# Kernel tuning notes

Hardware: AMD Instinct MI355X
Metric: run time of the kernel (lower is better)

The kernel has to match this reference:

```python
import jax, jax.numpy as jnp
import numpy as np
import math


def setup_inputs() -> dict:
    key = jax.random.key(0)
    k1, k2, k3 = jax.random.split(key, 3)
    B, L, H, E = 2, 2048, 8, 64
    queries = jax.random.normal(k1, (B, L, H, E), dtype=jnp.float32)
    keys = jax.random.normal(k2, (B, L, H, E), dtype=jnp.float32)
    values = jax.random.normal(k3, (B, L, H, E), dtype=jnp.float32)
    return {"queries": queries, "keys": keys, "values": values}


def reference(queries, keys, values):
    B, L, H, E = queries.shape
    scale = 1.0 / math.sqrt(E)
    # [B,H,L,S] attention scores
    scores = jnp.einsum('blhe,bshe->bhls', queries, keys)
    # causal mask: positions s > l masked to -inf (scale * -inf stays -inf)
    causal = jnp.triu(jnp.ones((L, L), dtype=bool), k=1)  # True above diagonal
    scores = jnp.where(causal[None, None, :, :], -jnp.inf, scores)
    attn = scale * scores
    SA = jax.nn.softmax(attn, axis=-1)  # dropout p=0.0 -> identity
    V = jnp.einsum('bhls,bshd->blhd', SA, values)
    return (V, SA)
```

## Files before the change

kernel.cpp:

```cpp
#include <hip/hip_runtime.h>
#include <math.h>

#define L_DIM 2048
#define H_DIM 8
#define ROWSTRIDE 512
#define NT 512
#define QSCALE 0.18033688011112042f

typedef __attribute__((ext_vector_type(8))) short short8;
typedef __attribute__((ext_vector_type(4))) float floatx4;

__device__ __forceinline__ unsigned short f2bf(float f) {
    unsigned int u = __builtin_bit_cast(unsigned int, f);
    return (unsigned short)((u + 0x8000u) >> 16);
}

__device__ __forceinline__ float fexp2(float x) {
#if __has_builtin(__builtin_amdgcn_exp2f)
    return __builtin_amdgcn_exp2f(x);
#else
    return exp2f(x);
#endif
}

__device__ __forceinline__ short8 pack8(float4 a, float4 b) {
    union { unsigned short us[8]; short8 v; } pk;
    pk.us[0]=f2bf(a.x); pk.us[1]=f2bf(a.y); pk.us[2]=f2bf(a.z); pk.us[3]=f2bf(a.w);
    pk.us[4]=f2bf(b.x); pk.us[5]=f2bf(b.y); pk.us[6]=f2bf(b.z); pk.us[7]=f2bf(b.w);
    return pk.v;
}

__device__ __forceinline__ short8 pack8q(float4 a, float4 b) {
    union { unsigned short us[8]; short8 v; } pk;
    pk.us[0]=f2bf(a.x*QSCALE); pk.us[1]=f2bf(a.y*QSCALE);
    pk.us[2]=f2bf(a.z*QSCALE); pk.us[3]=f2bf(a.w*QSCALE);
    pk.us[4]=f2bf(b.x*QSCALE); pk.us[5]=f2bf(b.y*QSCALE);
    pk.us[6]=f2bf(b.z*QSCALE); pk.us[7]=f2bf(b.w*QSCALE);
    return pk.v;
}

__device__ __forceinline__ int swz(int row, int col) {
    return (row << 6) + ((((col >> 3) ^ (row & 7)) << 3) | (col & 7));
}

__global__ __launch_bounds__(NT, 4)
void attn_mfma4(const float* __restrict__ Q, const float* __restrict__ K,
                const float* __restrict__ Vv, float* __restrict__ outV,
                float* __restrict__ outSA)
{
    __shared__ __align__(16) unsigned char smem[41984];
    unsigned short* Ks = (unsigned short*)(smem);
    unsigned short* Vt = (unsigned short*)(smem + 16384);
    unsigned short* Ps = (unsigned short*)(smem + 32768);
    float* Ml = (float*)(smem + 40960);
    float* Ll = (float*)(smem + 41472);
    float* Ob = (float*)(smem);

    const int t    = threadIdx.x;
    const int lane = t & 63;
    const int w    = t >> 6;
    const int g    = w >> 2;
    const int wg   = w & 3;
    const int l15  = lane & 15;
    const int quad = lane >> 4;
    const int gc   = g << 5;

    const int bid = blockIdx.x;
    const int c   = bid & 255;
    const int hf  = bid >> 8;
    const int bh  = c & 15;
    const int p   = c >> 4;
    const int qt  = hf ? p : (31 - p);
    const int h   = bh & 7;
    const int b   = bh >> 3;
    const int q0  = qt << 6;
    const int ntiles = qt + 1;

    const float* Qb = Q  + (size_t)b * L_DIM * ROWSTRIDE + h * 64;
    const float* Kb = K  + (size_t)b * L_DIM * ROWSTRIDE + h * 64;
    const float* Vb = Vv + (size_t)b * L_DIM * ROWSTRIDE + h * 64;
    float* saBase = outSA + (size_t)(b * H_DIM + h) * L_DIM * L_DIM;

    const int sr = t >> 3, sc = (t & 7) << 3;
    const int kswz = swz(sr, sc);

    short8 aQ0, aQ1;
    {
        const float* qsrc = Qb + (size_t)(q0 + 16 * wg + l15) * ROWSTRIDE + quad * 8;
        aQ0 = pack8q(*(const float4*)(qsrc),      *(const float4*)(qsrc + 4));
        aQ1 = pack8q(*(const float4*)(qsrc + 32), *(const float4*)(qsrc + 36));
    }

    float m_r[4], l_r[4];
#pragma unroll
    for (int r = 0; r < 4; ++r) { m_r[r] = -INFINITY; l_r[r] = 0.f; }

    {
        const float* src = Kb + (size_t)sr * ROWSTRIDE + sc;
        *(short8*)&Ks[kswz] = pack8(*(const float4*)src, *(const float4*)(src + 4));
    }
    __syncthreads();

    for (int st = 0; st < ntiles; ++st) {
        const int cur = st & 1;
        const int stp = (st + 1 < ntiles) ? (st + 1) : st;
        const float* ksrc = Kb + (size_t)((stp << 6) + sr) * ROWSTRIDE + sc;
        float4 kf0 = *(const float4*)(ksrc);
        float4 kf1 = *(const float4*)(ksrc + 4);

        const unsigned short* Kc = Ks + (cur << 12);
        floatx4 d[2];
#pragma unroll
        for (int jj = 0; jj < 2; ++jj) {
            const int sb = gc + (jj << 4) + l15;
            short8 b0 = *(const short8*)&Kc[swz(sb, quad * 8)];
            short8 b1 = *(const short8*)&Kc[swz(sb, 32 + quad * 8)];
            floatx4 acc = {0.f, 0.f, 0.f, 0.f};
            acc = __builtin_amdgcn_mfma_f32_16x16x32_bf16(aQ0, b0, acc, 0, 0, 0);
            acc = __builtin_amdgcn_mfma_f32_16x16x32_bf16(aQ1, b1, acc, 0, 0, 0);
            d[jj] = acc;
        }
        const int s0 = st << 6;
        const bool diag = (st == qt);
#pragma unroll
        for (int r = 0; r < 4; ++r) {
            const int lrow = q0 + 16 * wg + quad * 4 + r;
            float v0 = d[0][r], v1 = d[1][r];
            if (diag) {
                v0 = (s0 + gc +  0 + l15 <= lrow) ? v0 : -INFINITY;
                v1 = (s0 + gc + 16 + l15 <= lrow) ? v1 : -INFINITY;
            }
            float vm = fmaxf(v0, v1);
#pragma unroll
            for (int mk = 1; mk < 16; mk <<= 1) vm = fmaxf(vm, __shfl_xor(vm, mk));
            const float mnew = fmaxf(m_r[r], vm);
            const float msafe = (mnew == -INFINITY) ? 0.0f : mnew;
            float es = fexp2(v0 - msafe) + fexp2(v1 - msafe);
#pragma unroll
            for (int mk = 1; mk < 16; mk <<= 1) es += __shfl_xor(es, mk);
            l_r[r] = l_r[r] * fexp2(m_r[r] - msafe) + es;
            m_r[r] = mnew;
        }
        if (st + 1 < ntiles)
            *(short8*)&Ks[((cur ^ 1) << 12) + kswz] = pack8(kf0, kf1);
        __syncthreads();
    }

    if (l15 == 0) {
#pragma unroll
        for (int r = 0; r < 4; ++r) {
            const int row = 16 * wg + quad * 4 + r;
            Ml[g * 64 + row] = m_r[r];
            Ll[g * 64 + row] = l_r[r];
        }
    }
    {
        const float* src = Kb + (size_t)sr * ROWSTRIDE + sc;
        *(short8*)&Ks[kswz] = pack8(*(const float4*)src, *(const float4*)(src + 4));
        const float* vsrc = Vb + (size_t)sr * ROWSTRIDE + sc;
        float4 f0 = *(const float4*)(vsrc);
        float4 f1 = *(const float4*)(vsrc + 4);
        Vt[swz(sc + 0, sr)] = f2bf(f0.x); Vt[swz(sc + 1, sr)] = f2bf(f0.y);
        Vt[swz(sc + 2, sr)] = f2bf(f0.z); Vt[swz(sc + 3, sr)] = f2bf(f0.w);
        Vt[swz(sc + 4, sr)] = f2bf(f1.x); Vt[swz(sc + 5, sr)] = f2bf(f1.y);
        Vt[swz(sc + 6, sr)] = f2bf(f1.z); Vt[swz(sc + 7, sr)] = f2bf(f1.w);
    }
    __syncthreads();

    float mfin[4], invl[4];
#pragma unroll
    for (int r = 0; r < 4; ++r) {
        const int row = 16 * wg + quad * 4 + r;
        float m0 = Ml[row], m1 = Ml[64 + row];
        float l0 = Ll[row], l1 = Ll[64 + row];
        float mf = fmaxf(m0, m1);
        float lf = l0 * fexp2(m0 - mf) + l1 * fexp2(m1 - mf);
        mfin[r] = mf;
        invl[r] = 1.0f / lf;
    }

    floatx4 oacc[4];
#pragma unroll
    for (int j = 0; j < 4; ++j) oacc[j] = (floatx4){0.f, 0.f, 0.f, 0.f};

    for (int st = 0; st < ntiles; ++st) {
        const int cur = st & 1;
        const int stp = (st + 1 < ntiles) ? (st + 1) : st;
        const float* ksrc = Kb + (size_t)((stp << 6) + sr) * ROWSTRIDE + sc;
        const float* vsrc = Vb + (size_t)((stp << 6) + sr) * ROWSTRIDE + sc;
        float4 kf0 = *(const float4*)(ksrc);
        float4 kf1 = *(const float4*)(ksrc + 4);
        float4 vf0 = *(const float4*)(vsrc);
        float4 vf1 = *(const float4*)(vsrc + 4);

        const unsigned short* Kc = Ks + (cur << 12);
        floatx4 d[2];
#pragma unroll
        for (int jj = 0; jj < 2; ++jj) {
            const int sb = gc + (jj << 4) + l15;
            short8 b0 = *(const short8*)&Kc[swz(sb, quad * 8)];
            short8 b1 = *(const short8*)&Kc[swz(sb, 32 + quad * 8)];
            floatx4 acc = {0.f, 0.f, 0.f, 0.f};
            acc = __builtin_amdgcn_mfma_f32_16x16x32_bf16(aQ0, b0, acc, 0, 0, 0);
            acc = __builtin_amdgcn_mfma_f32_16x16x32_bf16(aQ1, b1, acc, 0, 0, 0);
            d[jj] = acc;
        }
        const int s0 = st << 6;
        const bool diag = (st == qt);
#pragma unroll
        for (int r = 0; r < 4; ++r) {
            const int lrow = q0 + 16 * wg + quad * 4 + r;
            float* sap = saBase + (size_t)lrow * L_DIM + s0 + gc + l15;
            const float mr = mfin[r], il = invl[r];
#pragma unroll
            for (int jj = 0; jj < 2; ++jj) {
                float v = d[jj][r];
                bool ok = !diag || (s0 + gc + 16 * jj + l15 <= lrow);
                float pv = ok ? fexp2(v - mr) * il : 0.0f;
                sap[16 * jj] = pv;
                Ps[swz(16 * wg + quad * 4 + r, gc + 16 * jj + l15)] = f2bf(pv);
            }
        }
        short8 aP = *(const short8*)&Ps[swz(16 * wg + l15, gc + quad * 8)];
        const unsigned short* Vc = Vt + (cur << 12);
#pragma unroll
        for (int j = 0; j < 4; ++j) {
            short8 bv = *(const short8*)&Vc[swz(16 * j + l15, gc + quad * 8)];
            oacc[j] = __builtin_amdgcn_mfma_f32_16x16x32_bf16(aP, bv, oacc[j], 0, 0, 0);
        }
        if (st + 1 < ntiles) {
            const int nb = (cur ^ 1) << 12;
            *(short8*)&Ks[nb + kswz] = pack8(kf0, kf1);
            unsigned short* Vn = Vt + nb;
            Vn[swz(sc + 0, sr)] = f2bf(vf0.x); Vn[swz(sc + 1, sr)] = f2bf(vf0.y);
            Vn[swz(sc + 2, sr)] = f2bf(vf0.z); Vn[swz(sc + 3, sr)] = f2bf(vf0.w);
            Vn[swz(sc + 4, sr)] = f2bf(vf1.x); Vn[swz(sc + 5, sr)] = f2bf(vf1.y);
            Vn[swz(sc + 6, sr)] = f2bf(vf1.z); Vn[swz(sc + 7, sr)] = f2bf(vf1.w);
        }
        __syncthreads();
    }

    if (g == 1) {
#pragma unroll
        for (int r = 0; r < 4; ++r) {
            const int row = 16 * wg + quad * 4 + r;
#pragma unroll
            for (int j = 0; j < 4; ++j)
                Ob[row * 65 + 16 * j + l15] = oacc[j][r];
        }
    }
    __syncthreads();
    if (g == 0) {
#pragma unroll
        for (int r = 0; r < 4; ++r) {
            const int row = 16 * wg + quad * 4 + r;
            float* op = outV + ((size_t)b * L_DIM + q0 + row) * ROWSTRIDE + h * 64 + l15;
#pragma unroll
            for (int j = 0; j < 4; ++j)
                op[16 * j] = oacc[j][r] + Ob[row * 65 + 16 * j + l15];
        }
    }

    {
        const int z0 = ntiles << 6;
        const int zr = t >> 3;
        float* rowp = saBase + (size_t)(q0 + zr) * L_DIM;
        const float4 zf = {0.f, 0.f, 0.f, 0.f};
        for (int s = z0 + (t & 7) * 4; s < L_DIM; s += 32)
            *(float4*)(rowp + s) = zf;
    }
}

extern "C" void kernel_launch(void* const* d_in, const int* in_sizes, int n_in,
                              void* d_out, int out_size, void* d_ws, size_t ws_size,
                              hipStream_t stream) {
    const float* Q  = (const float*)d_in[0];
    const float* K  = (const float*)d_in[1];
    const float* Vv = (const float*)d_in[2];
    float* out   = (float*)d_out;
    float* outV  = out;
    float* outSA = out + (size_t)2 * L_DIM * H_DIM * 64;

    dim3 grid(512);
    dim3 block(NT);
    attn_mfma4<<<grid, block, 0, stream>>>(Q, K, Vv, outV, outSA);
}
```

Before: 348.6 us.

## Defer softmax row reductions, fold normalizer into log, use packed bf16 converts

```diff
diff --git a/kernel.cpp b/kernel.cpp
--- a/kernel.cpp
+++ b/kernel.cpp
@@ -6,14 +6,10 @@
 #define ROWSTRIDE 512
 #define NT 512
 #define QSCALE 0.18033688011112042f
+#define FLT_BIG 3.402823466e+38f
 
 typedef __attribute__((ext_vector_type(8))) short short8;
 typedef __attribute__((ext_vector_type(4))) float floatx4;
-
-__device__ __forceinline__ unsigned short f2bf(float f) {
-    unsigned int u = __builtin_bit_cast(unsigned int, f);
-    return (unsigned short)((u + 0x8000u) >> 16);
-}
 
 __device__ __forceinline__ float fexp2(float x) {
 #if __has_builtin(__builtin_amdgcn_exp2f)
@@ -23,19 +19,33 @@
 #endif
 }
 
+__device__ __forceinline__ float flog2(float x) {
+#if __has_builtin(__builtin_amdgcn_logf)
+    return __builtin_amdgcn_logf(x);
+#else
+    return log2f(x);
+#endif
+}
+
+__device__ __forceinline__ unsigned int cvtpk(float lo, float hi) {
+    unsigned int r;
+    asm("v_cvt_pk_bf16_f32 %0, %1, %2" : "=v"(r) : "v"(lo), "v"(hi));
+    return r;
+}
+
 __device__ __forceinline__ short8 pack8(float4 a, float4 b) {
-    union { unsigned short us[8]; short8 v; } pk;
-    pk.us[0]=f2bf(a.x); pk.us[1]=f2bf(a.y); pk.us[2]=f2bf(a.z); pk.us[3]=f2bf(a.w);
-    pk.us[4]=f2bf(b.x); pk.us[5]=f2bf(b.y); pk.us[6]=f2bf(b.z); pk.us[7]=f2bf(b.w);
+    union { unsigned int u[4]; short8 v; } pk;
+    pk.u[0] = cvtpk(a.x, a.y); pk.u[1] = cvtpk(a.z, a.w);
+    pk.u[2] = cvtpk(b.x, b.y); pk.u[3] = cvtpk(b.z, b.w);
     return pk.v;
 }
 
 __device__ __forceinline__ short8 pack8q(float4 a, float4 b) {
-    union { unsigned short us[8]; short8 v; } pk;
-    pk.us[0]=f2bf(a.x*QSCALE); pk.us[1]=f2bf(a.y*QSCALE);
-    pk.us[2]=f2bf(a.z*QSCALE); pk.us[3]=f2bf(a.w*QSCALE);
-    pk.us[4]=f2bf(b.x*QSCALE); pk.us[5]=f2bf(b.y*QSCALE);
-    pk.us[6]=f2bf(b.z*QSCALE); pk.us[7]=f2bf(b.w*QSCALE);
+    union { unsigned int u[4]; short8 v; } pk;
+    pk.u[0] = cvtpk(a.x * QSCALE, a.y * QSCALE);
+    pk.u[1] = cvtpk(a.z * QSCALE, a.w * QSCALE);
+    pk.u[2] = cvtpk(b.x * QSCALE, b.y * QSCALE);
+    pk.u[3] = cvtpk(b.z * QSCALE, b.w * QSCALE);
     return pk.v;
 }
 
@@ -44,7 +54,7 @@
 }
 
 __global__ __launch_bounds__(NT, 4)
-void attn_mfma4(const float* __restrict__ Q, const float* __restrict__ K,
+void attn_mfma5(const float* __restrict__ Q, const float* __restrict__ K,
                 const float* __restrict__ Vv, float* __restrict__ outV,
                 float* __restrict__ outSA)
 {
@@ -93,7 +103,7 @@
 
     float m_r[4], l_r[4];
 #pragma unroll
-    for (int r = 0; r < 4; ++r) { m_r[r] = -INFINITY; l_r[r] = 0.f; }
+    for (int r = 0; r < 4; ++r) { m_r[r] = -FLT_BIG; l_r[r] = 0.f; }
 
     {
         const float* src = Kb + (size_t)sr * ROWSTRIDE + sc;
@@ -120,30 +130,43 @@
             acc = __builtin_amdgcn_mfma_f32_16x16x32_bf16(aQ1, b1, acc, 0, 0, 0);
             d[jj] = acc;
         }
-        const int s0 = st << 6;
-        const bool diag = (st == qt);
-#pragma unroll
-        for (int r = 0; r < 4; ++r) {
-            const int lrow = q0 + 16 * wg + quad * 4 + r;
-            float v0 = d[0][r], v1 = d[1][r];
-            if (diag) {
-                v0 = (s0 + gc +  0 + l15 <= lrow) ? v0 : -INFINITY;
-                v1 = (s0 + gc + 16 + l15 <= lrow) ? v1 : -INFINITY;
+        if (st == qt) {
+            const int s0 = st << 6;
+#pragma unroll
+            for (int r = 0; r < 4; ++r) {
+                const int lrow = q0 + 16 * wg + quad * 4 + r;
+                float v0 = (s0 + gc +  0 + l15 <= lrow) ? d[0][r] : -INFINITY;
+                float v1 = (s0 + gc + 16 + l15 <= lrow) ? d[1][r] : -INFINITY;
+                const float mnew = fmaxf(m_r[r], fmaxf(v0, v1));
+                float es = fexp2(v0 - mnew) + fexp2(v1 - mnew);
+                l_r[r] = l_r[r] * fexp2(m_r[r] - mnew) + es;
+                m_r[r] = mnew;
             }
-            float vm = fmaxf(v0, v1);
-#pragma unroll
-            for (int mk = 1; mk < 16; mk <<= 1) vm = fmaxf(vm, __shfl_xor(vm, mk));
-            const float mnew = fmaxf(m_r[r], vm);
-            const float msafe = (mnew == -INFINITY) ? 0.0f : mnew;
-            float es = fexp2(v0 - msafe) + fexp2(v1 - msafe);
-#pragma unroll
-            for (int mk = 1; mk < 16; mk <<= 1) es += __shfl_xor(es, mk);
-            l_r[r] = l_r[r] * fexp2(m_r[r] - msafe) + es;
-            m_r[r] = mnew;
+        } else {
+#pragma unroll
+            for (int r = 0; r < 4; ++r) {
+                float v0 = d[0][r], v1 = d[1][r];
+                const float mnew = fmaxf(m_r[r], fmaxf(v0, v1));
+                float es = fexp2(v0 - mnew) + fexp2(v1 - mnew);
+                l_r[r] = l_r[r] * fexp2(m_r[r] - mnew) + es;
+                m_r[r] = mnew;
+            }
         }
         if (st + 1 < ntiles)
             *(short8*)&Ks[((cur ^ 1) << 12) + kswz] = pack8(kf0, kf1);
         __syncthreads();
+    }
+
+#pragma unroll
+    for (int r = 0; r < 4; ++r) {
+#pragma unroll
+        for (int mk = 1; mk < 16; mk <<= 1) {
+            float mo = __shfl_xor(m_r[r], mk);
+            float lo = __shfl_xor(l_r[r], mk);
+            float mn = fmaxf(m_r[r], mo);
+            l_r[r] = l_r[r] * fexp2(m_r[r] - mn) + lo * fexp2(mo - mn);
+            m_r[r] = mn;
+        }
     }
 
     if (l15 == 0) {
@@ -160,14 +183,20 @@
         const float* vsrc = Vb + (size_t)sr * ROWSTRIDE + sc;
         float4 f0 = *(const float4*)(vsrc);
         float4 f1 = *(const float4*)(vsrc + 4);
-        Vt[swz(sc + 0, sr)] = f2bf(f0.x); Vt[swz(sc + 1, sr)] = f2bf(f0.y);
-        Vt[swz(sc + 2, sr)] = f2bf(f0.z); Vt[swz(sc + 3, sr)] = f2bf(f0.w);
-        Vt[swz(sc + 4, sr)] = f2bf(f1.x); Vt[swz(sc + 5, sr)] = f2bf(f1.y);
-        Vt[swz(sc + 6, sr)] = f2bf(f1.z); Vt[swz(sc + 7, sr)] = f2bf(f1.w);
+        unsigned int w01 = cvtpk(f0.x, f0.y), w23 = cvtpk(f0.z, f0.w);
+        unsigned int w45 = cvtpk(f1.x, f1.y), w67 = cvtpk(f1.z, f1.w);
+        Vt[swz(sc + 0, sr)] = (unsigned short)w01;
+        Vt[swz(sc + 1, sr)] = (unsigned short)(w01 >> 16);
+        Vt[swz(sc + 2, sr)] = (unsigned short)w23;
+        Vt[swz(sc + 3, sr)] = (unsigned short)(w23 >> 16);
+        Vt[swz(sc + 4, sr)] = (unsigned short)w45;
+        Vt[swz(sc + 5, sr)] = (unsigned short)(w45 >> 16);
+        Vt[swz(sc + 6, sr)] = (unsigned short)w67;
+        Vt[swz(sc + 7, sr)] = (unsigned short)(w67 >> 16);
     }
     __syncthreads();
 
-    float mfin[4], invl[4];
+    float c_r[4];
 #pragma unroll
     for (int r = 0; r < 4; ++r) {
         const int row = 16 * wg + quad * 4 + r;
@@ -175,8 +204,7 @@
         float l0 = Ll[row], l1 = Ll[64 + row];
         float mf = fmaxf(m0, m1);
         float lf = l0 * fexp2(m0 - mf) + l1 * fexp2(m1 - mf);
-        mfin[r] = mf;
-        invl[r] = 1.0f / lf;
+        c_r[r] = mf + flog2(lf);
     }
 
     floatx4 oacc[4];
@@ -206,19 +234,33 @@
             d[jj] = acc;
         }
         const int s0 = st << 6;
-        const bool diag = (st == qt);
-#pragma unroll
-        for (int r = 0; r < 4; ++r) {
-            const int lrow = q0 + 16 * wg + quad * 4 + r;
-            float* sap = saBase + (size_t)lrow * L_DIM + s0 + gc + l15;
-            const float mr = mfin[r], il = invl[r];
-#pragma unroll
-            for (int jj = 0; jj < 2; ++jj) {
-                float v = d[jj][r];
-                bool ok = !diag || (s0 + gc + 16 * jj + l15 <= lrow);
-                float pv = ok ? fexp2(v - mr) * il : 0.0f;
-                sap[16 * jj] = pv;
-                Ps[swz(16 * wg + quad * 4 + r, gc + 16 * jj + l15)] = f2bf(pv);
+        if (st == qt) {
+#pragma unroll
+            for (int r = 0; r < 4; ++r) {
+                const int lrow = q0 + 16 * wg + quad * 4 + r;
+                float* sap = saBase + (size_t)lrow * L_DIM + s0 + gc + l15;
+                const float cr = c_r[r];
+                float p0 = (s0 + gc +      l15 <= lrow) ? fexp2(d[0][r] - cr) : 0.0f;
+                float p1 = (s0 + gc + 16 + l15 <= lrow) ? fexp2(d[1][r] - cr) : 0.0f;
+                sap[0] = p0; sap[16] = p1;
+                unsigned int pw = cvtpk(p0, p1);
+                const int prow = 16 * wg + quad * 4 + r;
+                Ps[swz(prow, gc + l15)]      = (unsigned short)pw;
+                Ps[swz(prow, gc + 16 + l15)] = (unsigned short)(pw >> 16);
+            }
+        } else {
+#pragma unroll
+            for (int r = 0; r < 4; ++r) {
+                const int lrow = q0 + 16 * wg + quad * 4 + r;
+                float* sap = saBase + (size_t)lrow * L_DIM + s0 + gc + l15;
+                const float cr = c_r[r];
+                float p0 = fexp2(d[0][r] - cr);
+                float p1 = fexp2(d[1][r] - cr);
+                sap[0] = p0; sap[16] = p1;
+                unsigned int pw = cvtpk(p0, p1);
+                const int prow = 16 * wg + quad * 4 + r;
+                Ps[swz(prow, gc + l15)]      = (unsigned short)pw;
+                Ps[swz(prow, gc + 16 + l15)] = (unsigned short)(pw >> 16);
             }
         }
         short8 aP = *(const short8*)&Ps[swz(16 * wg + l15, gc + quad * 8)];
@@ -232,10 +274,16 @@
             const int nb = (cur ^ 1) << 12;
             *(short8*)&Ks[nb + kswz] = pack8(kf0, kf1);
             unsigned short* Vn = Vt + nb;
-            Vn[swz(sc + 0, sr)] = f2bf(vf0.x); Vn[swz(sc + 1, sr)] = f2bf(vf0.y);
-            Vn[swz(sc + 2, sr)] = f2bf(vf0.z); Vn[swz(sc + 3, sr)] = f2bf(vf0.w);
-            Vn[swz(sc + 4, sr)] = f2bf(vf1.x); Vn[swz(sc + 5, sr)] = f2bf(vf1.y);
-            Vn[swz(sc + 6, sr)] = f2bf(vf1.z); Vn[swz(sc + 7, sr)] = f2bf(vf1.w);
+            unsigned int w01 = cvtpk(vf0.x, vf0.y), w23 = cvtpk(vf0.z, vf0.w);
+            unsigned int w45 = cvtpk(vf1.x, vf1.y), w67 = cvtpk(vf1.z, vf1.w);
+            Vn[swz(sc + 0, sr)] = (unsigned short)w01;
+            Vn[swz(sc + 1, sr)] = (unsigned short)(w01 >> 16);
+            Vn[swz(sc + 2, sr)] = (unsigned short)w23;
+            Vn[swz(sc + 3, sr)] = (unsigned short)(w23 >> 16);
+            Vn[swz(sc + 4, sr)] = (unsigned short)w45;
+            Vn[swz(sc + 5, sr)] = (unsigned short)(w45 >> 16);
+            Vn[swz(sc + 6, sr)] = (unsigned short)w67;
+            Vn[swz(sc + 7, sr)] = (unsigned short)(w67 >> 16);
         }
         __syncthreads();
     }
@@ -283,5 +331,5 @@
 
     dim3 grid(512);
     dim3 block(NT);
-    attn_mfma4<<<grid, block, 0, stream>>>(Q, K, Vv, outV, outSA);
-}
+    attn_mfma5<<<grid, block, 0, stream>>>(Q, K, Vv, outV, outSA);
+}
```

Measured after the change: 330.5 us. 5.2% less time.
